# Optimization experiments

Hardware: AMD Instinct MI355X
Metric: run time of the kernel (lower is better)

Reference implementation:

```python
import jax, jax.numpy as jnp
import numpy as np

NUM_EMB = 1000
HIDDEN = 256
SCALE = 2
N_HEADS = 8
HEAD_DIM = HIDDEN * SCALE // N_HEADS  # 64
HS = HIDDEN * SCALE  # 512
EPS = 1e-6


def setup_inputs() -> dict:
    key = jax.random.key(0)
    ks = jax.random.split(key, 12)
    B, N, C, H, W = 8, 8, HIDDEN, 32, 32
    std = 0.02
    return {
        "q": jax.random.randint(ks[0], (B,), 0, NUM_EMB, dtype=jnp.int32),
        "c": jax.random.normal(ks[1], (B, N, C, H, W), dtype=jnp.float32),
        "rms_w": jnp.ones((HIDDEN,), dtype=jnp.float32),
        "emb": jax.random.normal(ks[2], (NUM_EMB, HIDDEN), dtype=jnp.float32) * std,
        "w1": jax.random.normal(ks[3], (HIDDEN, HS), dtype=jnp.float32) * std,
        "b1": jnp.zeros((HS,), dtype=jnp.float32),
        "w2": jax.random.normal(ks[4], (HS, HS), dtype=jnp.float32) * std,
        "b2": jnp.zeros((HS,), dtype=jnp.float32),
        "w_kv": jax.random.normal(ks[5], (HIDDEN, HS * 2), dtype=jnp.float32) * std,
        "w_out": jax.random.normal(ks[6], (HS, HIDDEN), dtype=jnp.float32) * std,
        "b_out": jnp.zeros((HIDDEN,), dtype=jnp.float32),
    }


def reference(q, c, rms_w, emb, w1, b1, w2, b2, w_kv, w_out, b_out):
    B, N, C, H, W = c.shape
    attn_scale = HEAD_DIM ** (-0.5)
    # permute to [B,H,W,N,C] and RMSNorm over channel dim
    c = jnp.transpose(c, (0, 3, 4, 1, 2))
    c = c * jax.lax.rsqrt(jnp.mean(c * c, axis=-1, keepdims=True) + EPS) * rms_w
    # query path: embed + gated MLP -> [B, n_heads, head_dim]
    qe = emb[q]                                   # [B, hidden]
    qh = jax.nn.silu(qe @ w1 + b1) @ w2 + b2      # [B, HS]
    qh = qh.reshape(B, N_HEADS, HEAD_DIM)
    # kv projection: [B,H,W,N, 2*HS] -> [B,H,W,n_heads,N, 2*head_dim]
    kv = (c @ w_kv).reshape(B, H, W, N, N_HEADS, 2 * HEAD_DIM)
    kv = jnp.transpose(kv, (0, 1, 2, 4, 3, 5))
    k, v = jnp.split(kv, 2, axis=-1)              # each [B,H,W,heads,N,head_dim]
    # broadcast per-pixel cross-attention: query shared over H,W
    dots = jnp.einsum('bed,bhwend->bhwen', qh, k) * attn_scale
    attn = jax.nn.softmax(dots, axis=-1)
    h = jnp.einsum('bhwen,bhwend->bhwed', attn, v)  # [B,H,W,heads,head_dim]
    h = h.reshape(B, H, W, HS)
    out = h @ w_out + b_out                        # [B,H,W,hidden]
    return jnp.transpose(out, (0, 3, 1, 2))        # [B,hidden,H,W]
```

## Files before the change

kernel.cpp:

```cpp
#include <hip/hip_runtime.h>

typedef _Float16 f16;
typedef _Float16 f16x4 __attribute__((ext_vector_type(4)));
typedef _Float16 f16x8 __attribute__((ext_vector_type(8)));
typedef float f32x4 __attribute__((ext_vector_type(4)));

static __device__ inline char* a_addr(char* Abase, int px, int k) {
    return Abase + px * 4096 + ((((k >> 3) ^ px) << 4) | ((k & 7) << 1));
}

__launch_bounds__(256)
__global__ void k_setup(const int* __restrict__ q, const float* __restrict__ emb,
                        const float* __restrict__ w1, const float* __restrict__ b1,
                        const float* __restrict__ w2, const float* __restrict__ b2,
                        const float* __restrict__ w_kv, const float* __restrict__ w_out,
                        const float* __restrict__ rms_w,
                        f16* __restrict__ qkw, f16* __restrict__ mtp) {
    int blk = blockIdx.x;
    int t = threadIdx.x;
    __shared__ float qe[256];
    __shared__ float x1L[512];
    __shared__ float ps[4][64];
    __shared__ float qhL[64];
    __shared__ float wv[64][8];

    if (blk < 64) {
        int b = blk >> 3, e = blk & 7;
        qe[t] = emb[(size_t)q[b] * 256 + t];
        __syncthreads();
        float a0 = b1[t], a1 = b1[t + 256];
#pragma unroll 4
        for (int c = 0; c < 256; ++c) {
            float qv = qe[c];
            a0 += qv * w1[c * 512 + t];
            a1 += qv * w1[c * 512 + t + 256];
        }
        x1L[t]       = a0 / (1.f + __expf(-a0));
        x1L[t + 256] = a1 / (1.f + __expf(-a1));
        __syncthreads();
        int d = t & 63, ks = t >> 6;
        float acc = 0.f;
#pragma unroll 4
        for (int k = ks * 128; k < ks * 128 + 128; ++k)
            acc += x1L[k] * w2[k * 512 + e * 64 + d];
        ps[ks][d] = acc;
        __syncthreads();
        if (t < 64)
            qhL[t] = b2[e * 64 + t] + ps[0][t] + ps[1][t] + ps[2][t] + ps[3][t];
        __syncthreads();
        const float* row = w_kv + (size_t)t * 1024 + e * 128;
        float a2 = 0.f;
#pragma unroll
        for (int dd = 0; dd < 64; dd += 4) {
            float4 wv4 = *(const float4*)(row + dd);
            a2 += qhL[dd] * wv4.x + qhL[dd + 1] * wv4.y + qhL[dd + 2] * wv4.z + qhL[dd + 3] * wv4.w;
        }
        qkw[(b * 8 + e) * 256 + t] = (f16)(a2 * rms_w[t]);
    } else {
        int mb = blk - 64;
        int e = mb >> 5, c0 = (mb & 31) * 8;
        {
            int d = t & 63, cc = t >> 6;
            wv[d][cc]     = w_kv[(size_t)(c0 + cc) * 1024 + e * 128 + 64 + d];
            wv[d][cc + 4] = w_kv[(size_t)(c0 + cc + 4) * 1024 + e * 128 + 64 + d];
        }
        __syncthreads();
        int o = t;
        float acc[8];
#pragma unroll
        for (int c = 0; c < 8; ++c) acc[c] = 0.f;
#pragma unroll 4
        for (int d = 0; d < 64; ++d) {
            float wo = w_out[(size_t)(e * 64 + d) * 256 + o];
            float4 wa = *(const float4*)&wv[d][0];
            float4 wb = *(const float4*)&wv[d][4];
            acc[0] += wa.x * wo; acc[1] += wa.y * wo; acc[2] += wa.z * wo; acc[3] += wa.w * wo;
            acc[4] += wb.x * wo; acc[5] += wb.y * wo; acc[6] += wb.z * wo; acc[7] += wb.w * wo;
        }
        f16x8 ov;
#pragma unroll
        for (int c = 0; c < 8; ++c) ov[c] = (f16)(acc[c] * rms_w[c0 + c]);
        *(f16x8*)(mtp + ((size_t)((e * 256 + c0) >> 3) * 256 + o) * 8) = ov;
    }
}

__launch_bounds__(512, 4)
__global__ void k_attn(const float* __restrict__ cin, const f16* __restrict__ qkw,
                       const f16* __restrict__ mtp, const float* __restrict__ b_out,
                       float* __restrict__ out) {
    int blk = blockIdx.x;
    int b = blk & 7;
    int hw0 = (blk >> 3) * 16;
    int t = threadIdx.x;
    int lane = t & 63, w = t >> 6;
    int m16 = lane & 15, quad = lane >> 4;

    __shared__ char A[16 * 4096];
    __shared__ float dotsP[8][8][16];
    __shared__ float wred[8][8][16];

    int px = t & 15, cb = t >> 4;
    const float* cbase = cin + ((size_t)b * 8 * 256) * 1024 + hw0 + px;
#pragma unroll
    for (int g = 0; g < 8; g += 2) {
        const float* s0 = cbase + ((size_t)(g * 256 + cb * 8) << 10);
        const float* s1 = cbase + ((size_t)((g + 1) * 256 + cb * 8) << 10);
        float v0[8], v1[8];
#pragma unroll
        for (int j = 0; j < 8; ++j) v0[j] = s0[(size_t)j << 10];
#pragma unroll
        for (int j = 0; j < 8; ++j) v1[j] = s1[(size_t)j << 10];
        float sa = 0.f, sb = 0.f;
        f16x8 h0, h1;
#pragma unroll
        for (int j = 0; j < 8; ++j) { sa += v0[j] * v0[j]; h0[j] = (f16)v0[j]; }
#pragma unroll
        for (int j = 0; j < 8; ++j) { sb += v1[j] * v1[j]; h1[j] = (f16)v1[j]; }
        *(f16x8*)a_addr(A, px, g * 256 + cb * 8)       = h0;
        *(f16x8*)a_addr(A, px, (g + 1) * 256 + cb * 8) = h1;
        sa += __shfl_xor(sa, 16); sa += __shfl_xor(sa, 32);
        sb += __shfl_xor(sb, 16); sb += __shfl_xor(sb, 32);
        if (lane < 16) {
            wred[w][g][px]     = sa;
            wred[w][g + 1][px] = sb;
        }
    }
    __syncthreads();

    {
        f32x4 d0 = {0.f, 0.f, 0.f, 0.f};
        const f16* qrow = qkw + (size_t)b * 2048 + (m16 & 7) * 256;
#pragma unroll
        for (int ks = 0; ks < 8; ++ks) {
            f16x8 a0  = *(const f16x8*)a_addr(A, m16, w * 256 + ks * 32 + quad * 8);
            f16x8 bfr = *(const f16x8*)(qrow + ks * 32 + quad * 8);
            d0 = __builtin_amdgcn_mfma_f32_16x16x32_f16(a0, bfr, d0, 0, 0, 0);
        }
        if (m16 < 8) {
#pragma unroll
            for (int r = 0; r < 4; ++r) dotsP[w][m16][quad * 4 + r] = d0[r];
        }
    }
    __syncthreads();

    f16x8 pb[4][2];
#pragma unroll
    for (int ks = 0; ks < 4; ++ks) {
        int kchunk = ks * 4 + quad;
#pragma unroll
        for (int ot = 0; ot < 2; ++ot)
            pb[ks][ot] = *(const f16x8*)(mtp + ((size_t)kchunk * 256
                                         + w * 32 + ot * 16 + m16) * 8);
    }

    {
        int bpx = t & 15, c0 = (t >> 4) * 8;
        float rinv[8];
#pragma unroll
        for (int n = 0; n < 8; ++n) {
            float ss = 0.f;
#pragma unroll
            for (int ww = 0; ww < 8; ++ww) ss += wred[ww][n][bpx];
            rinv[n] = rsqrtf(ss * (1.f / 256.f) + 1e-6f);
        }
        f16x8 cv[8];
#pragma unroll
        for (int n = 0; n < 8; ++n)
            cv[n] = *(const f16x8*)a_addr(A, bpx, n * 256 + c0);
#pragma unroll
        for (int e = 0; e < 8; ++e) {
            float l[8];
#pragma unroll
            for (int n = 0; n < 8; ++n) l[n] = dotsP[n][e][bpx] * rinv[n] * 0.125f;
            float mx = l[0];
#pragma unroll
            for (int n = 1; n < 8; ++n) mx = fmaxf(mx, l[n]);
            float s = 0.f;
#pragma unroll
            for (int n = 0; n < 8; ++n) { l[n] = __expf(l[n] - mx); s += l[n]; }
            float inv = 1.f / s;
            f16x8 r = {};
#pragma unroll
            for (int n = 0; n < 8; ++n) {
                f16 an = (f16)(l[n] * inv * rinv[n]);
#pragma unroll
                for (int j = 0; j < 8; ++j) r[j] += cv[n][j] * an;
            }
            *(f16x8*)a_addr(A, bpx, e * 256 + c0) = r;
        }
    }
    __syncthreads();

    {
        f32x4 acc[2];
        acc[0] = (f32x4){0.f, 0.f, 0.f, 0.f};
        acc[1] = (f32x4){0.f, 0.f, 0.f, 0.f};
#pragma unroll
        for (int ks = 0; ks < 4; ++ks) {
            f16x8 af = *(const f16x8*)a_addr(A, m16, ks * 32 + quad * 8);
            acc[0] = __builtin_amdgcn_mfma_f32_16x16x32_f16(af, pb[ks][0], acc[0], 0, 0, 0);
            acc[1] = __builtin_amdgcn_mfma_f32_16x16x32_f16(af, pb[ks][1], acc[1], 0, 0, 0);
        }
#pragma unroll 8
        for (int ks = 4; ks < 64; ++ks) {
            int k = (ks >> 3) * 256 + (ks & 7) * 32 + quad * 8;
            f16x8 af = *(const f16x8*)a_addr(A, m16, k);
            int kchunk = k >> 3;
#pragma unroll
            for (int ot = 0; ot < 2; ++ot) {
                f16x8 bfr = *(const f16x8*)(mtp + ((size_t)kchunk * 256
                                            + w * 32 + ot * 16 + m16) * 8);
                acc[ot] = __builtin_amdgcn_mfma_f32_16x16x32_f16(af, bfr, acc[ot], 0, 0, 0);
            }
        }
#pragma unroll
        for (int ot = 0; ot < 2; ++ot) {
            int o = w * 32 + ot * 16 + m16;
            float bo = b_out[o];
            float4 vv = {acc[ot][0] + bo, acc[ot][1] + bo, acc[ot][2] + bo, acc[ot][3] + bo};
            *(float4*)(out + ((size_t)b * 256 + o) * 1024 + hw0 + quad * 4) = vv;
        }
    }
}

extern "C" void kernel_launch(void* const* d_in, const int* in_sizes, int n_in,
                              void* d_out, int out_size, void* d_ws, size_t ws_size,
                              hipStream_t stream) {
    (void)in_sizes; (void)n_in; (void)out_size; (void)ws_size;
    const int*   q     = (const int*)d_in[0];
    const float* c     = (const float*)d_in[1];
    const float* rms_w = (const float*)d_in[2];
    const float* emb   = (const float*)d_in[3];
    const float* w1    = (const float*)d_in[4];
    const float* b1    = (const float*)d_in[5];
    const float* w2    = (const float*)d_in[6];
    const float* b2    = (const float*)d_in[7];
    const float* w_kv  = (const float*)d_in[8];
    const float* w_out = (const float*)d_in[9];
    const float* b_out = (const float*)d_in[10];
    float* out = (float*)d_out;

    char* ws = (char*)d_ws;
    f16* qkw = (f16*)ws;
    f16* mtp = (f16*)(ws + 32768);

    k_setup<<<320, 256, 0, stream>>>(q, emb, w1, b1, w2, b2, w_kv, w_out, rms_w, qkw, mtp);
    k_attn <<<512, 512, 0, stream>>>(c, qkw, mtp, b_out, out);
}
```

Measured before the change: 173.3 us.

## Process 32 pixels per block with 1024 threads to reuse output-weight fragments

The attention kernel now handles 32 pixels per block with 16 waves instead of 16 pixels with 8 waves, halving the grid. Each wave covers 16 output channels and two pixel tiles, so every weight fragment loaded from global memory feeds two MFMAs. The per-pixel RMS inverse is also computed once into shared memory rather than redundantly by every thread. In exchange, LDS per block doubles to about 140KB, leaving one block per CU, with 256 blocks for the whole device and less latency hiding between blocks.

```diff
diff --git a/kernel.cpp b/kernel.cpp
--- a/kernel.cpp
+++ b/kernel.cpp
@@ -1,12 +1,11 @@
 #include <hip/hip_runtime.h>
 
 typedef _Float16 f16;
-typedef _Float16 f16x4 __attribute__((ext_vector_type(4)));
 typedef _Float16 f16x8 __attribute__((ext_vector_type(8)));
 typedef float f32x4 __attribute__((ext_vector_type(4)));
 
 static __device__ inline char* a_addr(char* Abase, int px, int k) {
-    return Abase + px * 4096 + ((((k >> 3) ^ px) << 4) | ((k & 7) << 1));
+    return Abase + px * 4096 + ((((k >> 3) ^ (px & 15)) << 4) | ((k & 7) << 1));
 }
 
 __launch_bounds__(256)
@@ -84,22 +83,25 @@
     }
 }
 
-__launch_bounds__(512, 4)
+__launch_bounds__(1024, 4)
 __global__ void k_attn(const float* __restrict__ cin, const f16* __restrict__ qkw,
                        const f16* __restrict__ mtp, const float* __restrict__ b_out,
                        float* __restrict__ out) {
     int blk = blockIdx.x;
     int b = blk & 7;
-    int hw0 = (blk >> 3) * 16;
+    int hw0 = (blk >> 3) * 32;
     int t = threadIdx.x;
     int lane = t & 63, w = t >> 6;
     int m16 = lane & 15, quad = lane >> 4;
-
-    __shared__ char A[16 * 4096];
-    __shared__ float dotsP[8][8][16];
-    __shared__ float wred[8][8][16];
-
-    int px = t & 15, cb = t >> 4;
+    int half = lane >> 5;
+
+    __shared__ char A[32 * 4096];
+    __shared__ float dotsP[8][8][32];
+    __shared__ float wred[16][8][32];
+    __shared__ float rinvL[32][8];
+
+    int px = lane & 31;
+    int cb = w + half * 16;
     const float* cbase = cin + ((size_t)b * 8 * 256) * 1024 + hw0 + px;
 #pragma unroll
     for (int g = 0; g < 8; g += 2) {
@@ -118,51 +120,51 @@
         for (int j = 0; j < 8; ++j) { sb += v1[j] * v1[j]; h1[j] = (f16)v1[j]; }
         *(f16x8*)a_addr(A, px, g * 256 + cb * 8)       = h0;
         *(f16x8*)a_addr(A, px, (g + 1) * 256 + cb * 8) = h1;
-        sa += __shfl_xor(sa, 16); sa += __shfl_xor(sa, 32);
-        sb += __shfl_xor(sb, 16); sb += __shfl_xor(sb, 32);
-        if (lane < 16) {
+        sa += __shfl_xor(sa, 32);
+        sb += __shfl_xor(sb, 32);
+        if (lane < 32) {
             wred[w][g][px]     = sa;
             wred[w][g + 1][px] = sb;
         }
     }
     __syncthreads();
 
+    if (t < 256) {
+        int p = t >> 3, n = t & 7;
+        float ss = 0.f;
+#pragma unroll
+        for (int ww = 0; ww < 16; ++ww) ss += wred[ww][n][p];
+        rinvL[p][n] = rsqrtf(ss * (1.f / 256.f) + 1e-6f);
+    }
     {
+        int n = w & 7, pxh = w >> 3;
         f32x4 d0 = {0.f, 0.f, 0.f, 0.f};
         const f16* qrow = qkw + (size_t)b * 2048 + (m16 & 7) * 256;
 #pragma unroll
         for (int ks = 0; ks < 8; ++ks) {
-            f16x8 a0  = *(const f16x8*)a_addr(A, m16, w * 256 + ks * 32 + quad * 8);
+            f16x8 a0  = *(const f16x8*)a_addr(A, pxh * 16 + m16, n * 256 + ks * 32 + quad * 8);
             f16x8 bfr = *(const f16x8*)(qrow + ks * 32 + quad * 8);
             d0 = __builtin_amdgcn_mfma_f32_16x16x32_f16(a0, bfr, d0, 0, 0, 0);
         }
         if (m16 < 8) {
 #pragma unroll
-            for (int r = 0; r < 4; ++r) dotsP[w][m16][quad * 4 + r] = d0[r];
+            for (int r = 0; r < 4; ++r) dotsP[n][m16][pxh * 16 + quad * 4 + r] = d0[r];
         }
     }
     __syncthreads();
 
-    f16x8 pb[4][2];
-#pragma unroll
-    for (int ks = 0; ks < 4; ++ks) {
-        int kchunk = ks * 4 + quad;
-#pragma unroll
-        for (int ot = 0; ot < 2; ++ot)
-            pb[ks][ot] = *(const f16x8*)(mtp + ((size_t)kchunk * 256
-                                         + w * 32 + ot * 16 + m16) * 8);
-    }
+    int o = w * 16 + m16;
+    f16x8 pb[8];
+#pragma unroll
+    for (int ks = 0; ks < 8; ++ks)
+        pb[ks] = *(const f16x8*)(mtp + ((size_t)(ks * 4 + quad) * 256 + o) * 8);
 
     {
-        int bpx = t & 15, c0 = (t >> 4) * 8;
+        int bpx = lane & 31;
+        int c0 = (w + half * 16) * 8;
         float rinv[8];
 #pragma unroll
-        for (int n = 0; n < 8; ++n) {
-            float ss = 0.f;
-#pragma unroll
-            for (int ww = 0; ww < 8; ++ww) ss += wred[ww][n][bpx];
-            rinv[n] = rsqrtf(ss * (1.f / 256.f) + 1e-6f);
-        }
+        for (int n = 0; n < 8; ++n) rinv[n] = rinvL[bpx][n];
         f16x8 cv[8];
 #pragma unroll
         for (int n = 0; n < 8; ++n)
@@ -192,34 +194,32 @@
     __syncthreads();
 
     {
-        f32x4 acc[2];
-        acc[0] = (f32x4){0.f, 0.f, 0.f, 0.f};
-        acc[1] = (f32x4){0.f, 0.f, 0.f, 0.f};
-#pragma unroll
-        for (int ks = 0; ks < 4; ++ks) {
-            f16x8 af = *(const f16x8*)a_addr(A, m16, ks * 32 + quad * 8);
-            acc[0] = __builtin_amdgcn_mfma_f32_16x16x32_f16(af, pb[ks][0], acc[0], 0, 0, 0);
-            acc[1] = __builtin_amdgcn_mfma_f32_16x16x32_f16(af, pb[ks][1], acc[1], 0, 0, 0);
+        f32x4 acc0 = {0.f, 0.f, 0.f, 0.f};
+        f32x4 acc1 = {0.f, 0.f, 0.f, 0.f};
+#pragma unroll
+        for (int ks = 0; ks < 8; ++ks) {
+            int k = ks * 32 + quad * 8;
+            f16x8 af0 = *(const f16x8*)a_addr(A, m16, k);
+            f16x8 af1 = *(const f16x8*)a_addr(A, m16 + 16, k);
+            acc0 = __builtin_amdgcn_mfma_f32_16x16x32_f16(af0, pb[ks], acc0, 0, 0, 0);
+            acc1 = __builtin_amdgcn_mfma_f32_16x16x32_f16(af1, pb[ks], acc1, 0, 0, 0);
         }
 #pragma unroll 8
-        for (int ks = 4; ks < 64; ++ks) {
+        for (int ks = 8; ks < 64; ++ks) {
             int k = (ks >> 3) * 256 + (ks & 7) * 32 + quad * 8;
-            f16x8 af = *(const f16x8*)a_addr(A, m16, k);
             int kchunk = k >> 3;
-#pragma unroll
-            for (int ot = 0; ot < 2; ++ot) {
-                f16x8 bfr = *(const f16x8*)(mtp + ((size_t)kchunk * 256
-                                            + w * 32 + ot * 16 + m16) * 8);
-                acc[ot] = __builtin_amdgcn_mfma_f32_16x16x32_f16(af, bfr, acc[ot], 0, 0, 0);
-            }
-        }
-#pragma unroll
-        for (int ot = 0; ot < 2; ++ot) {
-            int o = w * 32 + ot * 16 + m16;
-            float bo = b_out[o];
-            float4 vv = {acc[ot][0] + bo, acc[ot][1] + bo, acc[ot][2] + bo, acc[ot][3] + bo};
-            *(float4*)(out + ((size_t)b * 256 + o) * 1024 + hw0 + quad * 4) = vv;
-        }
+            f16x8 bfr = *(const f16x8*)(mtp + ((size_t)kchunk * 256 + o) * 8);
+            f16x8 af0 = *(const f16x8*)a_addr(A, m16, k);
+            f16x8 af1 = *(const f16x8*)a_addr(A, m16 + 16, k);
+            acc0 = __builtin_amdgcn_mfma_f32_16x16x32_f16(af0, bfr, acc0, 0, 0, 0);
+            acc1 = __builtin_amdgcn_mfma_f32_16x16x32_f16(af1, bfr, acc1, 0, 0, 0);
+        }
+        float bo = b_out[o];
+        float* drow = out + ((size_t)b * 256 + o) * 1024 + hw0;
+        float4 v0 = {acc0[0] + bo, acc0[1] + bo, acc0[2] + bo, acc0[3] + bo};
+        float4 v1 = {acc1[0] + bo, acc1[1] + bo, acc1[2] + bo, acc1[3] + bo};
+        *(float4*)(drow + quad * 4)      = v0;
+        *(float4*)(drow + 16 + quad * 4) = v1;
     }
 }
 
@@ -245,5 +245,5 @@
     f16* mtp = (f16*)(ws + 32768);
 
     k_setup<<<320, 256, 0, stream>>>(q, emb, w1, b1, w2, b2, w_kv, w_out, rms_w, qkw, mtp);
-    k_attn <<<512, 512, 0, stream>>>(c, qkw, mtp, b_out, out);
-}
+    k_attn <<<256, 1024, 0, stream>>>(c, qkw, mtp, b_out, out);
+}
```

Result: faster. 167.1 us (-3.6%).
